# Optimization experiments

Measured on AMD Instinct MI355X. Metric: run time of the kernel, lower is better.

## Reference

```python
import jax, jax.numpy as jnp
import numpy as np

SEQ = 2048
D_MODEL = 2048
N_HEAD = 16
D_QK = 128
D_V = 128


def setup_inputs() -> dict:
    key = jax.random.key(0)
    ks = jax.random.split(key, 5)
    return {
        "x": jax.random.normal(ks[0], (SEQ, D_MODEL), dtype=jnp.float32),
        "q": jax.random.normal(ks[1], (N_HEAD, D_MODEL, D_QK), dtype=jnp.float32),
        "k": jax.random.normal(ks[2], (N_HEAD, D_MODEL, D_QK), dtype=jnp.float32),
        "v": jax.random.normal(ks[3], (N_HEAD, D_MODEL, D_V), dtype=jnp.float32),
        "o": jax.random.normal(ks[4], (N_HEAD, D_V, D_MODEL), dtype=jnp.float32),
        "theta_factor": jnp.asarray(10000.0, dtype=jnp.float32),
    }


def _rope_embed(x, theta_factor, d_qk):
    # x: [n_head, seq, d_qk]; faithful to source: rate is LINEAR in theta_factor
    seq = x.shape[1]
    d_rope = d_qk // 2
    rate = theta_factor * (-jnp.arange(d_rope, dtype=x.dtype) / d_rope)  # [d_rope]
    pos = jnp.arange(seq, dtype=x.dtype)                                 # [seq]
    rot = pos[:, None] * rate[None, :]                                   # [seq, d_rope]
    sin, cos = jnp.sin(rot), jnp.cos(rot)
    x1, x2 = x[..., :d_rope], x[..., d_rope:]
    y = jnp.concatenate([cos * x1 - sin * x2, sin * x1 + cos * x2], axis=-1)
    return y / d_qk ** 0.25  # qk_layer_norm is None path


def reference(x, q, k, v, o, theta_factor):
    seq, d_model = x.shape
    n_head, _, d_qk = q.shape
    d_v = v.shape[2]
    scale = 1.0 / jnp.sqrt(jnp.asarray(n_head * d_v * d_model, dtype=x.dtype))
    # causal mask: (tril - 1) * 1e9, as in source
    mask = (jnp.tril(jnp.ones((seq, seq), dtype=x.dtype)) - 1.0) * 1e9
    # per-head projections (vmapped heads expressed as einsum over h)
    rq = _rope_embed(jnp.einsum('sd,hde->hse', x, q), theta_factor, d_qk)
    rk = _rope_embed(jnp.einsum('sd,hde->hse', x, k), theta_factor, d_qk)
    vs = jnp.einsum('sd,hdv->hsv', x, v)
    scores = jnp.einsum('hse,hte->hst', rq, rk) + mask  # [h, s, s]
    w = jax.nn.softmax(scores, axis=-1)
    y = jnp.einsum('hst,htv->hsv', w, vs)
    z = jnp.einsum('hsv,hvd->sd', y, o)
    return z * scale
```

## Files before the change

### kernel.cpp

```cpp
#include <hip/hip_runtime.h>
#include <math.h>


typedef _Float16 half_t;
typedef __attribute__((ext_vector_type(8))) _Float16 half8;
typedef __attribute__((ext_vector_type(4))) float f32x4;

#define SEQ   2048
#define DM    2048
#define NHEAD 16

__device__ __forceinline__ f32x4 mfma16(half8 a, half8 b, f32x4 c) {
  return __builtin_amdgcn_mfma_f32_16x16x32_f16(a, b, c, 0, 0, 0);
}

__device__ __forceinline__ void gll16(const half_t* g, half_t* l) {
  __builtin_amdgcn_global_load_lds(
      (const __attribute__((address_space(1))) unsigned int*)g,
      (__attribute__((address_space(3))) unsigned int*)l, 16, 0, 0);
}

template <int CTRL>
__device__ __forceinline__ float dppf(float v) {
  int r = __builtin_amdgcn_mov_dpp(__builtin_bit_cast(int, v), CTRL, 0xF, 0xF,
                                   true);
  return __builtin_bit_cast(float, r);
}
__device__ __forceinline__ float red16_max(float v) {
  v = fmaxf(v, dppf<0xB1>(v));
  v = fmaxf(v, dppf<0x4E>(v));
  v = fmaxf(v, dppf<0x141>(v));
  v = fmaxf(v, dppf<0x140>(v));
  return v;
}
__device__ __forceinline__ float red16_sum(float v) {
  v += dppf<0xB1>(v);
  v += dppf<0x4E>(v);
  v += dppf<0x141>(v);
  v += dppf<0x140>(v);
  return v;
}

__device__ __forceinline__ void tpose32(const float* __restrict__ in,
                                        half_t* __restrict__ hi,
                                        half_t* __restrict__ lo, int R, int C,
                                        int r0, int c0, float (*tile)[33],
                                        int tid) {
  int tx = tid & 31, ty = tid >> 5;
#pragma unroll
  for (int i = 0; i < 32; i += 8)
    tile[ty + i][tx] = in[(size_t)(r0 + ty + i) * C + c0 + tx];
  __syncthreads();
#pragma unroll
  for (int i = 0; i < 32; i += 8) {
    float v = tile[tx][ty + i];
    half_t h = (half_t)v;
    size_t oidx = (size_t)(c0 + ty + i) * R + r0 + tx;
    hi[oidx] = h;
    if (lo) lo[oidx] = (half_t)(v - (float)h);
  }
}

__global__ __launch_bounds__(256)
void k_pre(const float* __restrict__ x, const float* __restrict__ q,
           const float* __restrict__ k, const float* __restrict__ v,
           const float* __restrict__ o, const float* __restrict__ thetap,
           half_t* __restrict__ Xh, half_t* __restrict__ Xl,
           half_t* __restrict__ WTh, half_t* __restrict__ WTl,
           half_t* __restrict__ VhT, half_t* __restrict__ OT,
           float2* __restrict__ trig) {
  __shared__ float tile[32][33];
  int b = blockIdx.x, tid = threadIdx.x;
  if (b < 4096) {
    int i = b * 256 + tid;
    float4 vv = ((const float4*)x)[i];
    union { half_t h[4]; uint2 u; } H, L;
    H.h[0] = (half_t)vv.x; H.h[1] = (half_t)vv.y;
    H.h[2] = (half_t)vv.z; H.h[3] = (half_t)vv.w;
    L.h[0] = (half_t)(vv.x - (float)H.h[0]);
    L.h[1] = (half_t)(vv.y - (float)H.h[1]);
    L.h[2] = (half_t)(vv.z - (float)H.h[2]);
    L.h[3] = (half_t)(vv.w - (float)H.h[3]);
    *(uint2*)&Xh[(size_t)i * 4] = H.u;
    *(uint2*)&Xl[(size_t)i * 4] = L.u;
  } else if (b < 16384) {
    int j = b - 4096;
    int which = j >> 12, z = (j >> 8) & 15, tb = j & 255;
    int c0 = (tb & 3) * 32, r0 = (tb >> 2) * 32;
    const float* src =
        (which == 0 ? q : which == 1 ? k : v) + (size_t)z * 2048 * 128;
    size_t doff = (size_t)z * 128 * 2048;
    if (which == 0)
      tpose32(src, WTh + doff, WTl + doff, 2048, 128, r0, c0, tile, tid);
    else if (which == 1) {
      size_t koff = (size_t)16 * 128 * 2048 + doff;
      tpose32(src, WTh + koff, WTl + koff, 2048, 128, r0, c0, tile, tid);
    } else
      tpose32(src, VhT + doff, nullptr, 2048, 128, r0, c0, tile, tid);
  } else if (b < 20480) {
    int j = b - 16384;
    int c0 = (j & 63) * 32, r0 = (j >> 6) * 32;
    tpose32(o, OT, nullptr, 2048, 2048, r0, c0, tile, tid);
  } else {
    int idx = (b - 20480) * 256 + tid;
    int s = idx >> 6, e = idx & 63;
    float th = thetap[0];
    float rate = th * (-(float)e * (1.0f / 64.0f));
    float rot = (float)s * rate;
    double rev = (double)rot * 0.15915494309189535;
    double fr = rev - rint(rev);
    float thr = (float)(fr * 6.283185307179586);
    float sn = sinf(thr), cs = cosf(thr);
    const float inv4 = 0.2973017787506803f;
    trig[idx] = make_float2(cs * inv4, sn * inv4);
  }
}

__global__ __launch_bounds__(256, 2)
void k_proj(const half_t* __restrict__ Xh, const half_t* __restrict__ Xl,
            const half_t* __restrict__ WTh, const half_t* __restrict__ WTl,
            const float2* __restrict__ trig, half_t* __restrict__ Rh,
            half_t* __restrict__ Rl) {
  __shared__ __align__(16) char smem[65536];
  half_t* sAh = (half_t*)smem;
  half_t* sAl = (half_t*)(smem + 16384);
  half_t* sBh = (half_t*)(smem + 32768);
  half_t* sBl = (half_t*)(smem + 49152);
  int y = blockIdx.y;
  int m0 = blockIdx.x * 128;
  const half_t* wth = WTh + (size_t)y * 128 * DM;
  const half_t* wtl = WTl + (size_t)y * 128 * DM;
  int lane = threadIdx.x & 63, wave = threadIdx.x >> 6;
  int l15 = lane & 15, quad = lane >> 4;
  int wm = wave >> 1, wn = wave & 1;

  f32x4 acc[4][4];
#pragma unroll
  for (int a = 0; a < 4; ++a)
#pragma unroll
    for (int b = 0; b < 4; ++b) acc[a][b] = (f32x4)0.0f;

  for (int kt = 0; kt < DM / 64; ++kt) {
    int k0 = kt * 64;
#pragma unroll
    for (int i = 0; i < 4; ++i) {
      int c = wave * 4 + i;
      int g = c * 64 + lane;
      int row = g >> 3;
      int lc = (g & 7) ^ (row & 7);
      size_t ro = (size_t)row * DM + k0 + lc * 8;
      gll16(Xh + (size_t)m0 * DM + ro, sAh + c * 512);
      gll16(Xl + (size_t)m0 * DM + ro, sAl + c * 512);
      gll16(wth + ro, sBh + c * 512);
      gll16(wtl + ro, sBl + c * 512);
    }
    __syncthreads();
#pragma unroll
    for (int kk = 0; kk < 2; ++kk) {
      half8 ah[4], al[4], bh[4], bl[4];
#pragma unroll
      for (int t = 0; t < 4; ++t) {
        int ar = wm * 64 + t * 16 + l15;
        int br = wn * 64 + t * 16 + l15;
        int ao = ar * 64 + (((kk * 4 + quad) ^ (ar & 7)) * 8);
        int bo = br * 64 + (((kk * 4 + quad) ^ (br & 7)) * 8);
        ah[t] = *(const half8*)&sAh[ao];
        al[t] = *(const half8*)&sAl[ao];
        bh[t] = *(const half8*)&sBh[bo];
        bl[t] = *(const half8*)&sBl[bo];
      }
#pragma unroll
      for (int im = 0; im < 4; ++im)
#pragma unroll
        for (int in = 0; in < 4; ++in) {
          acc[im][in] = mfma16(ah[im], bh[in], acc[im][in]);
          acc[im][in] = mfma16(ah[im], bl[in], acc[im][in]);
          acc[im][in] = mfma16(al[im], bh[in], acc[im][in]);
        }
    }
    __syncthreads();
  }
  float* tile = (float*)smem;
  size_t ybase = (size_t)y * SEQ * 128;
#pragma unroll
  for (int p = 0; p < 2; ++p) {
    if (p) __syncthreads();
    if (wm == p) {
#pragma unroll
      for (int im = 0; im < 4; ++im)
#pragma unroll
        for (int in = 0; in < 4; ++in)
#pragma unroll
          for (int r = 0; r < 4; ++r)
            tile[(im * 16 + quad * 4 + r) * 132 + wn * 64 + in * 16 + l15] =
                acc[im][in][r];
    }
    __syncthreads();
    int e = lane;
#pragma unroll 4
    for (int rr = 0; rr < 16; ++rr) {
      int rloc = wave * 16 + rr;
      int s = m0 + p * 64 + rloc;
      float x1 = tile[rloc * 132 + e];
      float x2 = tile[rloc * 132 + 64 + e];
      float2 sc = trig[s * 64 + e];
      float y1 = sc.x * x1 - sc.y * x2;
      float y2 = sc.y * x1 + sc.x * x2;
      half_t h1 = (half_t)y1, h2 = (half_t)y2;
      size_t base = ybase + (size_t)s * 128;
      Rh[base + e] = h1;       Rl[base + e] = (half_t)(y1 - (float)h1);
      Rh[base + 64 + e] = h2;  Rl[base + 64 + e] = (half_t)(y2 - (float)h2);
    }
  }
}

template <int HALF_OUT>
__global__ __launch_bounds__(256)
void k_gemm1(const half_t* __restrict__ A, const half_t* __restrict__ B,
             void* __restrict__ Cv, float scale) {
  __shared__ __align__(16) half_t sA[64 * 64], sB[128 * 64];
  int lin = blockIdx.y * 16 + blockIdx.x;
  int xcd = lin & 7, slot = lin >> 3;
  int bx = (xcd & 3) * 4 + (slot & 3);
  int by = (xcd >> 2) * 16 + (slot >> 2);
  int am0 = by * 64, bn0 = bx * 128;
  int lane = threadIdx.x & 63, wave = threadIdx.x >> 6;
  int l15 = lane & 15, quad = lane >> 4;
  int wm = wave >> 1, wn = wave & 1;

  f32x4 acc[2][4];
#pragma unroll
  for (int a = 0; a < 2; ++a)
#pragma unroll
    for (int b = 0; b < 4; ++b) acc[a][b] = (f32x4)0.0f;

  for (int kt = 0; kt < DM / 64; ++kt) {
    int k0 = kt * 64;
#pragma unroll
    for (int i = 0; i < 2; ++i) {
      int g0 = (i * 4 + wave) * 64;
      int g = g0 + lane;
      int row = g >> 3;
      int lc = (g & 7) ^ (row & 7);
      gll16(A + (size_t)(am0 + row) * 2048 + k0 + lc * 8, sA + g0 * 8);
    }
#pragma unroll
    for (int i = 0; i < 4; ++i) {
      int g0 = (i * 4 + wave) * 64;
      int g = g0 + lane;
      int row = g >> 3;
      int lc = (g & 7) ^ (row & 7);
      gll16(B + (size_t)(bn0 + row) * 2048 + k0 + lc * 8, sB + g0 * 8);
    }
    __syncthreads();
#pragma unroll
    for (int kk = 0; kk < 2; ++kk) {
      half8 ah[2], bh[4];
#pragma unroll
      for (int t = 0; t < 2; ++t) {
        int ar = wm * 32 + t * 16 + l15;
        ah[t] = *(const half8*)&sA[ar * 64 + (((kk * 4 + quad) ^ (ar & 7)) * 8)];
      }
#pragma unroll
      for (int t = 0; t < 4; ++t) {
        int br = wn * 64 + t * 16 + l15;
        bh[t] = *(const half8*)&sB[br * 64 + (((kk * 4 + quad) ^ (br & 7)) * 8)];
      }
#pragma unroll
      for (int im = 0; im < 2; ++im)
#pragma unroll
        for (int in = 0; in < 4; ++in)
          acc[im][in] = mfma16(ah[im], bh[in], acc[im][in]);
    }
    __syncthreads();
  }
#pragma unroll
  for (int im = 0; im < 2; ++im)
#pragma unroll
    for (int in = 0; in < 4; ++in)
#pragma unroll
      for (int r = 0; r < 4; ++r) {
        int row = am0 + wm * 32 + im * 16 + quad * 4 + r;
        int col = bn0 + wn * 64 + in * 16 + l15;
        if (HALF_OUT)
          ((half_t*)Cv)[(size_t)row * 2048 + col] = (half_t)(acc[im][in][r] * scale);
        else
          ((float*)Cv)[(size_t)row * 2048 + col] = acc[im][in][r] * scale;
      }
}

__global__ __launch_bounds__(256, 2)
void k_flash(const half_t* __restrict__ Rh, const half_t* __restrict__ Rl,
             const half_t* __restrict__ VST, half_t* __restrict__ Ybig) {
  int idx = blockIdx.x;
  int h = idx & 15;
  int qt = (idx < 256) ? (31 - (idx >> 4)) : ((idx - 256) >> 4);
  int lane = threadIdx.x & 63, wave = threadIdx.x >> 6;
  int l15 = lane & 15, quad = lane >> 4;

  const half_t* RQh = Rh + (size_t)h * SEQ * 128;
  const half_t* RQl = Rl + (size_t)h * SEQ * 128;
  const half_t* RKh = Rh + (size_t)(NHEAD + h) * SEQ * 128;
  const half_t* RKl = Rl + (size_t)(NHEAD + h) * SEQ * 128;
  const half_t* Vt  = VST + (size_t)h * 128 * SEQ;

  __shared__ __align__(16) half_t sKh[64 * 128];
  __shared__ __align__(16) half_t sKl[64 * 128];
  __shared__ __align__(16) half_t sVt[128 * 64];
  __shared__ __align__(16) half_t sP[64 * 72];

  int q0 = qt * 64;

  half8 qh[4], ql[4];
#pragma unroll
  for (int kk = 0; kk < 4; ++kk) {
    size_t ad = (size_t)(q0 + wave * 16 + l15) * 128 + kk * 32 + quad * 8;
    qh[kk] = *(const half8*)&RQh[ad];
    ql[kk] = *(const half8*)&RQl[ad];
  }

  int rk_r = (lane >> 4);
  int rv_r = (lane >> 3);

  float4 pk0, pk1, pk2, pk3, pl0, pl1, pl2, pl3, pv0, pv1, pv2, pv3;

#define FL_ONE(i, t0)                                                     \
  {                                                                       \
    int c = wave * 4 + i;                                                 \
    int rk = c * 4 + rk_r;                                                \
    int ck = (lane & 15) ^ (rk & 15);                                     \
    pk##i = *(const float4*)(RKh + (size_t)((t0) + rk) * 128 + ck * 8);   \
    pl##i = *(const float4*)(RKl + (size_t)((t0) + rk) * 128 + ck * 8);   \
    int rv = c * 8 + rv_r;                                                \
    int cv = (lane & 7) ^ (rv & 7);                                       \
    pv##i = *(const float4*)(Vt + (size_t)rv * SEQ + (t0) + cv * 8);      \
  }
#define FLOAD(t0) FL_ONE(0, t0) FL_ONE(1, t0) FL_ONE(2, t0) FL_ONE(3, t0)

#define FW_ONE(i)                                                         \
  {                                                                       \
    int c = wave * 4 + i;                                                 \
    *(float4*)(sKh + c * 512 + lane * 8) = pk##i;                         \
    *(float4*)(sKl + c * 512 + lane * 8) = pl##i;                         \
    *(float4*)(sVt + c * 512 + lane * 8) = pv##i;                         \
  }
#define FWRITE() FW_ONE(0) FW_ONE(1) FW_ONE(2) FW_ONE(3)

  float m_st[4], l_st[4];
  f32x4 oacc[8];
#pragma unroll
  for (int r = 0; r < 4; ++r) { m_st[r] = -INFINITY; l_st[r] = 0.0f; }
#pragma unroll
  for (int iv = 0; iv < 8; ++iv) oacc[iv] = (f32x4)0.0f;

  int nkb = qt + 1;
  FLOAD(0);
  for (int kb = 0; kb < nkb; ++kb) {
    FWRITE();
    if (kb + 1 < nkb) FLOAD((kb + 1) * 64);
    asm volatile("s_waitcnt lgkmcnt(0)" ::: "memory");
    __builtin_amdgcn_s_barrier();

    f32x4 sacc[4];
#pragma unroll
    for (int in = 0; in < 4; ++in) sacc[in] = (f32x4)0.0f;
#pragma unroll
    for (int kk = 0; kk < 4; ++kk)
#pragma unroll
      for (int in = 0; in < 4; ++in) {
        int bo = (in * 16 + l15) * 128 + (((kk * 4 + quad) ^ l15) * 8);
        half8 bh = *(const half8*)&sKh[bo];
        half8 bl = *(const half8*)&sKl[bo];
        sacc[in] = mfma16(qh[kk], bh, sacc[in]);
        sacc[in] = mfma16(qh[kk], bl, sacc[in]);
        sacc[in] = mfma16(ql[kk], bh, sacc[in]);
      }
    if (kb == qt) {
#pragma unroll
      for (int in = 0; in < 4; ++in)
#pragma unroll
        for (int r = 0; r < 4; ++r)
          if (in * 16 + l15 > wave * 16 + quad * 4 + r) sacc[in][r] = -1e30f;
    }
    float alpha[4];
#pragma unroll
    for (int r = 0; r < 4; ++r) {
      float mx = fmaxf(fmaxf(sacc[0][r], sacc[1][r]),
                       fmaxf(sacc[2][r], sacc[3][r]));
      mx = red16_max(mx);
      float mnew = fmaxf(m_st[r], mx);
      alpha[r] = __expf(m_st[r] - mnew);
      float sum = 0.0f;
#pragma unroll
      for (int in = 0; in < 4; ++in) {
        float p = __expf(sacc[in][r] - mnew);
        sacc[in][r] = p;
        sum += p;
      }
      sum = red16_sum(sum);
      l_st[r] = l_st[r] * alpha[r] + sum;
      m_st[r] = mnew;
    }
#pragma unroll
    for (int in = 0; in < 4; ++in)
#pragma unroll
      for (int r = 0; r < 4; ++r)
        sP[(wave * 16 + quad * 4 + r) * 72 + in * 16 + l15] =
            (half_t)sacc[in][r];
#pragma unroll
    for (int iv = 0; iv < 8; ++iv)
#pragma unroll
      for (int r = 0; r < 4; ++r) oacc[iv][r] *= alpha[r];

#pragma unroll
    for (int kk2 = 0; kk2 < 2; ++kk2) {
      half8 pa =
          *(const half8*)&sP[(wave * 16 + l15) * 72 + kk2 * 32 + quad * 8];
#pragma unroll
      for (int iv = 0; iv < 8; ++iv) {
        half8 vb = *(const half8*)&sVt[(iv * 16 + l15) * 64 +
                                       (((kk2 * 4 + quad) ^ (l15 & 7)) * 8)];
        oacc[iv] = mfma16(pa, vb, oacc[iv]);
      }
    }
    asm volatile("" ::: "memory");
    __builtin_amdgcn_s_barrier();
  }
  float invl[4];
#pragma unroll
  for (int r = 0; r < 4; ++r) invl[r] = 1.0f / l_st[r];
#pragma unroll
  for (int iv = 0; iv < 8; ++iv)
#pragma unroll
    for (int r = 0; r < 4; ++r) {
      int row = q0 + wave * 16 + quad * 4 + r;
      int col = h * 128 + iv * 16 + l15;
      Ybig[(size_t)row * 2048 + col] = (half_t)(oacc[iv][r] * invl[r]);
    }
#undef FL_ONE
#undef FLOAD
#undef FW_ONE
#undef FWRITE
}

extern "C" void kernel_launch(void* const* d_in, const int* in_sizes, int n_in,
                              void* d_out, int out_size, void* d_ws,
                              size_t ws_size, hipStream_t stream) {
  const float* x = (const float*)d_in[0];
  const float* q = (const float*)d_in[1];
  const float* k = (const float*)d_in[2];
  const float* v = (const float*)d_in[3];
  const float* o = (const float*)d_in[4];
  const float* theta = (const float*)d_in[5];
  float* out = (float*)d_out;

  char* ws = (char*)d_ws;
  const size_t HB = (size_t)2048 * 2048 * 2;
  half_t* Xh   = (half_t*)(ws);
  half_t* Xl   = (half_t*)(ws + HB);
  half_t* WTh  = (half_t*)(ws + 2 * HB);
  half_t* WTl  = (half_t*)(ws + 4 * HB);
  half_t* VhT  = (half_t*)(ws + 6 * HB);
  half_t* OT   = (half_t*)(ws + 7 * HB);
  half_t* Rh   = (half_t*)(ws + 8 * HB);
  half_t* Rl   = (half_t*)(ws + 10 * HB);
  float2* trig = (float2*)(ws + 12 * HB);
  half_t* VST  = (half_t*)(ws + 2 * HB);
  half_t* Ybig = (half_t*)(ws + 3 * HB);

  k_pre<<<20992, 256, 0, stream>>>(x, q, k, v, o, theta, Xh, Xl, WTh, WTl,
                                   VhT, OT, trig);
  k_proj<<<dim3(16, 32), 256, 0, stream>>>(Xh, Xl, WTh, WTl, trig, Rh, Rl);
  k_gemm1<1><<<dim3(16, 32), 256, 0, stream>>>(VhT, Xh, VST, 1.0f);
  k_flash<<<512, 256, 0, stream>>>(Rh, Rl, VST, Ybig);
  k_gemm1<0><<<dim3(16, 32), 256, 0, stream>>>(Ybig, OT, out, 1.0f / 2048.0f);
}
```

Measured before the change: 339.6 us.

## Merge Q/K projection and V projection into one heterogeneous kernel launch

Combines the RoPE Q/K projection GEMM and the V projection GEMM into a single launch of 1024 blocks, interleaving the two kinds of block in groups of eight. This lets the lighter V GEMM blocks fill the tail of the heavier split-precision projection blocks, and it removes one kernel boundary. VST moves to a separate workspace region because it can no longer alias the WT buffers while those are still being read. The cost is a kernel that needs the register and shared-memory budget of the larger branch, which may limit occupancy for the V-GEMM blocks.

```diff
diff --git a/kernel.cpp b/kernel.cpp
--- a/kernel.cpp
+++ b/kernel.cpp
@@ -117,100 +117,171 @@
 }
 
 __global__ __launch_bounds__(256, 2)
-void k_proj(const half_t* __restrict__ Xh, const half_t* __restrict__ Xl,
-            const half_t* __restrict__ WTh, const half_t* __restrict__ WTl,
-            const float2* __restrict__ trig, half_t* __restrict__ Rh,
-            half_t* __restrict__ Rl) {
+void k_fused(const half_t* __restrict__ Xh, const half_t* __restrict__ Xl,
+             const half_t* __restrict__ WTh, const half_t* __restrict__ WTl,
+             const float2* __restrict__ trig, half_t* __restrict__ Rh,
+             half_t* __restrict__ Rl, const half_t* __restrict__ VhT,
+             half_t* __restrict__ VST) {
   __shared__ __align__(16) char smem[65536];
-  half_t* sAh = (half_t*)smem;
-  half_t* sAl = (half_t*)(smem + 16384);
-  half_t* sBh = (half_t*)(smem + 32768);
-  half_t* sBl = (half_t*)(smem + 49152);
-  int y = blockIdx.y;
-  int m0 = blockIdx.x * 128;
-  const half_t* wth = WTh + (size_t)y * 128 * DM;
-  const half_t* wtl = WTl + (size_t)y * 128 * DM;
+  int lin = blockIdx.x;
+  int grp = (lin >> 3) & 1;
+  int id = (lin >> 4) * 8 + (lin & 7);
   int lane = threadIdx.x & 63, wave = threadIdx.x >> 6;
   int l15 = lane & 15, quad = lane >> 4;
   int wm = wave >> 1, wn = wave & 1;
 
-  f32x4 acc[4][4];
-#pragma unroll
-  for (int a = 0; a < 4; ++a)
-#pragma unroll
-    for (int b = 0; b < 4; ++b) acc[a][b] = (f32x4)0.0f;
-
-  for (int kt = 0; kt < DM / 64; ++kt) {
-    int k0 = kt * 64;
-#pragma unroll
-    for (int i = 0; i < 4; ++i) {
-      int c = wave * 4 + i;
-      int g = c * 64 + lane;
-      int row = g >> 3;
-      int lc = (g & 7) ^ (row & 7);
-      size_t ro = (size_t)row * DM + k0 + lc * 8;
-      gll16(Xh + (size_t)m0 * DM + ro, sAh + c * 512);
-      gll16(Xl + (size_t)m0 * DM + ro, sAl + c * 512);
-      gll16(wth + ro, sBh + c * 512);
-      gll16(wtl + ro, sBl + c * 512);
-    }
-    __syncthreads();
-#pragma unroll
-    for (int kk = 0; kk < 2; ++kk) {
-      half8 ah[4], al[4], bh[4], bl[4];
-#pragma unroll
-      for (int t = 0; t < 4; ++t) {
-        int ar = wm * 64 + t * 16 + l15;
-        int br = wn * 64 + t * 16 + l15;
-        int ao = ar * 64 + (((kk * 4 + quad) ^ (ar & 7)) * 8);
-        int bo = br * 64 + (((kk * 4 + quad) ^ (br & 7)) * 8);
-        ah[t] = *(const half8*)&sAh[ao];
-        al[t] = *(const half8*)&sAl[ao];
-        bh[t] = *(const half8*)&sBh[bo];
-        bl[t] = *(const half8*)&sBl[bo];
-      }
-#pragma unroll
-      for (int im = 0; im < 4; ++im)
-#pragma unroll
-        for (int in = 0; in < 4; ++in) {
-          acc[im][in] = mfma16(ah[im], bh[in], acc[im][in]);
-          acc[im][in] = mfma16(ah[im], bl[in], acc[im][in]);
-          acc[im][in] = mfma16(al[im], bh[in], acc[im][in]);
+  if (grp == 0) {
+    half_t* sAh = (half_t*)smem;
+    half_t* sAl = (half_t*)(smem + 16384);
+    half_t* sBh = (half_t*)(smem + 32768);
+    half_t* sBl = (half_t*)(smem + 49152);
+    int y = id >> 4;
+    int m0 = (id & 15) * 128;
+    const half_t* wth = WTh + (size_t)y * 128 * DM;
+    const half_t* wtl = WTl + (size_t)y * 128 * DM;
+
+    f32x4 acc[4][4];
+#pragma unroll
+    for (int a = 0; a < 4; ++a)
+#pragma unroll
+      for (int b = 0; b < 4; ++b) acc[a][b] = (f32x4)0.0f;
+
+    for (int kt = 0; kt < DM / 64; ++kt) {
+      int k0 = kt * 64;
+#pragma unroll
+      for (int i = 0; i < 4; ++i) {
+        int c = wave * 4 + i;
+        int g = c * 64 + lane;
+        int row = g >> 3;
+        int lc = (g & 7) ^ (row & 7);
+        size_t ro = (size_t)row * DM + k0 + lc * 8;
+        gll16(Xh + (size_t)m0 * DM + ro, sAh + c * 512);
+        gll16(Xl + (size_t)m0 * DM + ro, sAl + c * 512);
+        gll16(wth + ro, sBh + c * 512);
+        gll16(wtl + ro, sBl + c * 512);
+      }
+      __syncthreads();
+#pragma unroll
+      for (int kk = 0; kk < 2; ++kk) {
+        half8 ah[4], al[4], bh[4], bl[4];
+#pragma unroll
+        for (int t = 0; t < 4; ++t) {
+          int ar = wm * 64 + t * 16 + l15;
+          int br = wn * 64 + t * 16 + l15;
+          int ao = ar * 64 + (((kk * 4 + quad) ^ (ar & 7)) * 8);
+          int bo = br * 64 + (((kk * 4 + quad) ^ (br & 7)) * 8);
+          ah[t] = *(const half8*)&sAh[ao];
+          al[t] = *(const half8*)&sAl[ao];
+          bh[t] = *(const half8*)&sBh[bo];
+          bl[t] = *(const half8*)&sBl[bo];
         }
-    }
-    __syncthreads();
-  }
-  float* tile = (float*)smem;
-  size_t ybase = (size_t)y * SEQ * 128;
-#pragma unroll
-  for (int p = 0; p < 2; ++p) {
-    if (p) __syncthreads();
-    if (wm == p) {
-#pragma unroll
-      for (int im = 0; im < 4; ++im)
-#pragma unroll
-        for (int in = 0; in < 4; ++in)
-#pragma unroll
-          for (int r = 0; r < 4; ++r)
-            tile[(im * 16 + quad * 4 + r) * 132 + wn * 64 + in * 16 + l15] =
-                acc[im][in][r];
-    }
-    __syncthreads();
-    int e = lane;
+#pragma unroll
+        for (int im = 0; im < 4; ++im)
+#pragma unroll
+          for (int in = 0; in < 4; ++in) {
+            acc[im][in] = mfma16(ah[im], bh[in], acc[im][in]);
+            acc[im][in] = mfma16(ah[im], bl[in], acc[im][in]);
+            acc[im][in] = mfma16(al[im], bh[in], acc[im][in]);
+          }
+      }
+      __syncthreads();
+    }
+    float* tile = (float*)smem;
+    size_t ybase = (size_t)y * SEQ * 128;
+#pragma unroll
+    for (int p = 0; p < 2; ++p) {
+      if (p) __syncthreads();
+      if (wm == p) {
+#pragma unroll
+        for (int im = 0; im < 4; ++im)
+#pragma unroll
+          for (int in = 0; in < 4; ++in)
+#pragma unroll
+            for (int r = 0; r < 4; ++r)
+              tile[(im * 16 + quad * 4 + r) * 132 + wn * 64 + in * 16 + l15] =
+                  acc[im][in][r];
+      }
+      __syncthreads();
+      int e = lane;
 #pragma unroll 4
-    for (int rr = 0; rr < 16; ++rr) {
-      int rloc = wave * 16 + rr;
-      int s = m0 + p * 64 + rloc;
-      float x1 = tile[rloc * 132 + e];
-      float x2 = tile[rloc * 132 + 64 + e];
-      float2 sc = trig[s * 64 + e];
-      float y1 = sc.x * x1 - sc.y * x2;
-      float y2 = sc.y * x1 + sc.x * x2;
-      half_t h1 = (half_t)y1, h2 = (half_t)y2;
-      size_t base = ybase + (size_t)s * 128;
-      Rh[base + e] = h1;       Rl[base + e] = (half_t)(y1 - (float)h1);
-      Rh[base + 64 + e] = h2;  Rl[base + 64 + e] = (half_t)(y2 - (float)h2);
-    }
+      for (int rr = 0; rr < 16; ++rr) {
+        int rloc = wave * 16 + rr;
+        int s = m0 + p * 64 + rloc;
+        float x1 = tile[rloc * 132 + e];
+        float x2 = tile[rloc * 132 + 64 + e];
+        float2 sc = trig[s * 64 + e];
+        float y1 = sc.x * x1 - sc.y * x2;
+        float y2 = sc.y * x1 + sc.x * x2;
+        half_t h1 = (half_t)y1, h2 = (half_t)y2;
+        size_t base = ybase + (size_t)s * 128;
+        Rh[base + e] = h1;       Rl[base + e] = (half_t)(y1 - (float)h1);
+        Rh[base + 64 + e] = h2;  Rl[base + 64 + e] = (half_t)(y2 - (float)h2);
+      }
+    }
+  } else {
+    half_t* sA = (half_t*)smem;
+    half_t* sB = (half_t*)(smem + 8192);
+    int xcd = id & 7, slot = id >> 3;
+    int bx = (xcd & 3) * 4 + (slot & 3);
+    int by = (xcd >> 2) * 16 + (slot >> 2);
+    int am0 = by * 64, bn0 = bx * 128;
+
+    f32x4 acc[2][4];
+#pragma unroll
+    for (int a = 0; a < 2; ++a)
+#pragma unroll
+      for (int b = 0; b < 4; ++b) acc[a][b] = (f32x4)0.0f;
+
+    for (int kt = 0; kt < DM / 64; ++kt) {
+      int k0 = kt * 64;
+#pragma unroll
+      for (int i = 0; i < 2; ++i) {
+        int g0 = (i * 4 + wave) * 64;
+        int g = g0 + lane;
+        int row = g >> 3;
+        int lc = (g & 7) ^ (row & 7);
+        gll16(VhT + (size_t)(am0 + row) * 2048 + k0 + lc * 8, sA + g0 * 8);
+      }
+#pragma unroll
+      for (int i = 0; i < 4; ++i) {
+        int g0 = (i * 4 + wave) * 64;
+        int g = g0 + lane;
+        int row = g >> 3;
+        int lc = (g & 7) ^ (row & 7);
+        gll16(Xh + (size_t)(bn0 + row) * 2048 + k0 + lc * 8, sB + g0 * 8);
+      }
+      __syncthreads();
+#pragma unroll
+      for (int kk = 0; kk < 2; ++kk) {
+        half8 ah[2], bh[4];
+#pragma unroll
+        for (int t = 0; t < 2; ++t) {
+          int ar = wm * 32 + t * 16 + l15;
+          ah[t] = *(const half8*)&sA[ar * 64 + (((kk * 4 + quad) ^ (ar & 7)) * 8)];
+        }
+#pragma unroll
+        for (int t = 0; t < 4; ++t) {
+          int br = wn * 64 + t * 16 + l15;
+          bh[t] = *(const half8*)&sB[br * 64 + (((kk * 4 + quad) ^ (br & 7)) * 8)];
+        }
+#pragma unroll
+        for (int im = 0; im < 2; ++im)
+#pragma unroll
+          for (int in = 0; in < 4; ++in)
+            acc[im][in] = mfma16(ah[im], bh[in], acc[im][in]);
+      }
+      __syncthreads();
+    }
+#pragma unroll
+    for (int im = 0; im < 2; ++im)
+#pragma unroll
+      for (int in = 0; in < 4; ++in)
+#pragma unroll
+        for (int r = 0; r < 4; ++r) {
+          int row = am0 + wm * 32 + im * 16 + quad * 4 + r;
+          int col = bn0 + wn * 64 + in * 16 + l15;
+          VST[(size_t)row * 2048 + col] = (half_t)acc[im][in][r];
+        }
   }
 }
 
@@ -465,13 +536,12 @@
   half_t* Rh   = (half_t*)(ws + 8 * HB);
   half_t* Rl   = (half_t*)(ws + 10 * HB);
   float2* trig = (float2*)(ws + 12 * HB);
-  half_t* VST  = (half_t*)(ws + 2 * HB);
+  half_t* VST  = (half_t*)(ws + 13 * HB);
   half_t* Ybig = (half_t*)(ws + 3 * HB);
 
   k_pre<<<20992, 256, 0, stream>>>(x, q, k, v, o, theta, Xh, Xl, WTh, WTl,
                                    VhT, OT, trig);
-  k_proj<<<dim3(16, 32), 256, 0, stream>>>(Xh, Xl, WTh, WTl, trig, Rh, Rl);
-  k_gemm1<1><<<dim3(16, 32), 256, 0, stream>>>(VhT, Xh, VST, 1.0f);
+  k_fused<<<1024, 256, 0, stream>>>(Xh, Xl, WTh, WTl, trig, Rh, Rl, VhT, VST);
   k_flash<<<512, 256, 0, stream>>>(Rh, Rl, VST, Ybig);
   k_gemm1<0><<<dim3(16, 32), 256, 0, stream>>>(Ybig, OT, out, 1.0f / 2048.0f);
 }
```

Result: slower. 375.5 us (+10.6%).
